# Optimization experiments

Measured on AMD Instinct MI355X. Metric: run time of the kernel, lower is better.

Reference implementation:

```python
import jax, jax.numpy as jnp
import numpy as np

B, H, W, C, NH, WS = 8, 113, 113, 512, 8, 7


def setup_inputs() -> dict:
    key = jax.random.key(0)
    k1, k2, k3 = jax.random.split(key, 3)
    x = jax.random.normal(k1, (B, H * W, C), jnp.float32)
    # torch Linear(embed_dims, 3*embed_dims, bias=False); stored as [C, 3C] for x @ W
    w_qkv = jax.random.normal(k2, (C, 3 * C), jnp.float32) * 0.02
    w_proj = jax.random.normal(k3, (C, C), jnp.float32) * 0.02
    b_proj = jnp.zeros((C,), jnp.float32)
    return {"x": x, "w_qkv": w_qkv, "w_proj": w_proj, "b_proj": b_proj, "h": H, "w": W}


def reference(x, w_qkv, w_proj, b_proj, h, w):
    b, n, c = x.shape
    ws, nh = WS, NH
    hd = c // nh
    scale = hd ** -0.5
    pad_b = (ws - h % ws) % ws
    pad_r = (ws - w % ws) % ws
    xi = x.reshape(b, h, w, c)
    xi = jnp.pad(xi, ((0, 0), (0, pad_b), (0, pad_r), (0, 0)))
    Hp, Wp = h + pad_b, w + pad_r
    _h, _w = Hp // ws, Wp // ws
    N = ws * ws
    nw = _h * _w

    # padding mask: 1 on padded rows/cols (matches torch fill of last pad_b rows / pad_r cols;
    # when pad==0 torch fills everything with 1 but mask differences are identically 0 either way)
    rows = jnp.arange(Hp)
    cols = jnp.arange(Wp)
    mask = ((rows[:, None] >= Hp - pad_b) | (cols[None, :] >= Wp - pad_r)).astype(x.dtype)
    mask = mask.reshape(_h, ws, _w, ws).transpose(0, 2, 1, 3).reshape(nw, N)
    am = mask[:, None, :] - mask[:, :, None]  # (nw, N, N)
    am = jnp.where(am != 0, jnp.asarray(-1000.0, x.dtype), jnp.asarray(0.0, x.dtype))

    # window partition: (b, _h, _w, ws, ws, c) -> (b, nw, N, c)
    xw = xi.reshape(b, _h, ws, _w, ws, c).transpose(0, 1, 3, 2, 4, 5).reshape(b, nw, N, c)

    qkv = (xw @ w_qkv).reshape(b, nw, N, 3, nh, hd)
    qkv = jnp.moveaxis(qkv, 3, 0)  # (3, b, nw, N, nh, hd)
    q = qkv[0].transpose(0, 1, 3, 2, 4)  # (b, nw, nh, N, hd)
    k = qkv[1].transpose(0, 1, 3, 2, 4)
    v = qkv[2].transpose(0, 1, 3, 2, 4)

    attn = jnp.einsum('bwhnd,bwhmd->bwhnm', q, k) * scale
    attn = attn + am[None, :, None, :, :]
    attn = jax.nn.softmax(attn, axis=-1)
    out = jnp.einsum('bwhnm,bwhmd->bwhnd', attn, v)  # (b, nw, nh, N, hd)

    # window merge back to (b, Hp, Wp, c)
    out = out.transpose(0, 1, 3, 2, 4).reshape(b, _h, _w, ws, ws, c)
    out = out.transpose(0, 1, 3, 2, 4, 5).reshape(b, Hp, Wp, c)
    out = out[:, :h, :w, :].reshape(b, n, c)
    return out @ w_proj + b_proj
```

## Files before the change

### kernel.cpp

```cpp
#include <hip/hip_runtime.h>
#include <hip/hip_fp16.h>
#include <stdint.h>

typedef _Float16 f16;
typedef __attribute__((ext_vector_type(4))) _Float16 f16x4;
typedef __attribute__((ext_vector_type(8))) _Float16 f16x8;
typedef __attribute__((ext_vector_type(4))) float f32x4;

#define DEVI static __device__ __forceinline__

#define C_DIM 512
#define M1    113288
#define M2    102152
#define NWIN  289
#define NTOK  49
#define NHW   18496
#define QKV_STRIDE 3136

DEVI void load_lds16(const f16* g, f16* l) {
  __builtin_amdgcn_global_load_lds((const __attribute__((address_space(1))) void*)g,
                                   (__attribute__((address_space(3))) void*)l,
                                   16, 0, 0);
}

DEVI f32x4 mfma_16x16x32(f16x8 a, f16x8 b, f32x4 c) {
  return __builtin_amdgcn_mfma_f32_16x16x32_f16(a, b, c, 0, 0, 0);
}

__global__ void cvt_x_kernel(const float* __restrict__ x, f16* __restrict__ xh,
                             f16* __restrict__ zp) {
  if (blockIdx.x == 0 && threadIdx.x < 64) {
    ((int4*)zp)[threadIdx.x] = make_int4(0, 0, 0, 0);
  }
  const int n8 = 6537728;
  int i = blockIdx.x * blockDim.x + threadIdx.x;
  for (; i < n8; i += gridDim.x * blockDim.x) {
    const float4* p = (const float4*)(x) + (size_t)i * 2;
    const float4 a = p[0], b = p[1];
    f16x8 o;
    o[0] = (f16)a.x; o[1] = (f16)a.y; o[2] = (f16)a.z; o[3] = (f16)a.w;
    o[4] = (f16)b.x; o[5] = (f16)b.y; o[6] = (f16)b.z; o[7] = (f16)b.w;
    *(f16x8*)(xh + (size_t)i * 8) = o;
  }
}

__global__ void cvt_wT_kernel(const float* __restrict__ w, f16* __restrict__ wt,
                              int K, int N) {
  const int i = blockIdx.x * blockDim.x + threadIdx.x;
  if (i < K * N) {
    const int n = i / K;
    const int k = i - n * K;
    wt[i] = (f16)w[(size_t)k * N + n];
  }
}

template<int MODE>
__global__ __launch_bounds__(256, 2)
void gemm_kernel(const f16* __restrict__ A, const f16* __restrict__ Bt,
                 f16* __restrict__ qo, f16* __restrict__ ko, f16* __restrict__ vo,
                 float* __restrict__ out, const float* __restrict__ bias,
                 const f16* __restrict__ zp)
{
  __shared__ __align__(16) f16 S[16384];
  f16* As = S;
  f16* Bs = S + 8192;

  const int tid  = threadIdx.x;
  const int wave = tid >> 6;
  const int lane = tid & 63;
  const int l16  = lane & 15;
  const int g    = lane >> 4;

  constexpr int NTN = (MODE == 0) ? 12 : 4;
  const int nwg = gridDim.x;
  const int qq = nwg >> 3, rr = nwg & 7;
  const int xcd = blockIdx.x & 7, ib = blockIdx.x >> 3;
  const int wg = (xcd < rr ? xcd * (qq + 1) : rr * (qq + 1) + (xcd - rr) * qq) + ib;
  const int tn = wg % NTN;
  const int tm = wg / NTN;

  const int srow  = tid >> 3;
  const int chunk = tid & 7;
  const int lc    = chunk ^ (srow & 7);
  const f16* asrc[4];
  const f16* bsrc[4];
  #pragma unroll
  for (int c = 0; c < 4; ++c) {
    const int m = tm * 128 + c * 32 + srow;
    long src = 0; bool valid;
    if (MODE == 0) {
      const int b   = m / 14161;
      const int rem = m - b * 14161;
      const int wi  = rem / 49;
      const int t   = rem - wi * 49;
      const int wh = wi / 17, ww = wi - (wi / 17) * 17;
      const int th = t / 7,   tw = t - (t / 7) * 7;
      const int h = wh * 7 + th, w = ww * 7 + tw;
      valid = (m < M1) && (h < 113) && (w < 113);
      src = (long)b * 12769 + h * 113 + w;
    } else {
      const int b = m / 12769;
      const int p = m - b * 12769;
      const int h = p / 113, w = p - (p / 113) * 113;
      valid = (m < M2);
      src = (long)((b * NWIN + (h / 7) * 17 + (w / 7)) * NTOK + (h % 7) * 7 + (w % 7));
    }
    asrc[c] = valid ? (A + src * C_DIM + lc * 8) : zp;
    bsrc[c] = Bt + (long)(tn * 128 + c * 32 + srow) * C_DIM + lc * 8;
  }

  int aoff[4], boff[4];
  #pragma unroll
  for (int i = 0; i < 4; ++i) {
    const int ra = (wave >> 1) * 64 + 16 * i + l16;
    aoff[i] = ra * 128 + ((g ^ (l16 & 7)) << 4);
    const int rb = (wave & 1) * 64 + 16 * i + l16;
    boff[i] = rb * 128 + ((g ^ (l16 & 7)) << 4);
  }

  f32x4 acc[4][4];
  #pragma unroll
  for (int i = 0; i < 4; ++i)
    #pragma unroll
    for (int j = 0; j < 4; ++j)
      acc[i][j] = (f32x4){0.f, 0.f, 0.f, 0.f};

  for (int kk = 0; kk < 8; ++kk) {
    __syncthreads();
    #pragma unroll
    for (int c = 0; c < 4; ++c) {
      load_lds16(asrc[c], &As[c * 2048 + wave * 512]);
      asrc[c] += 64;
    }
    #pragma unroll
    for (int c = 0; c < 4; ++c) {
      load_lds16(bsrc[c], &Bs[c * 2048 + wave * 512]);
      bsrc[c] += 64;
    }
    __syncthreads();

    #pragma unroll
    for (int kh = 0; kh < 2; ++kh) {
      f16x8 af[4], bf[4];
      #pragma unroll
      for (int i = 0; i < 4; ++i) af[i] = *(const f16x8*)((const char*)As + (aoff[i] ^ (kh << 6)));
      #pragma unroll
      for (int j = 0; j < 4; ++j) bf[j] = *(const f16x8*)((const char*)Bs + (boff[j] ^ (kh << 6)));
      #pragma unroll
      for (int i = 0; i < 4; ++i)
        #pragma unroll
        for (int j = 0; j < 4; ++j)
          acc[i][j] = mfma_16x16x32(af[i], bf[j], acc[i][j]);
    }
  }

  if (MODE == 0) {
    __syncthreads();
    char* Cs = (char*)S;
    const int rw0 = (wave >> 1) * 64 + g * 4;
    const int cl0 = (wave & 1) * 64 + l16;
    #pragma unroll
    for (int i = 0; i < 4; ++i) {
      #pragma unroll
      for (int rg = 0; rg < 4; ++rg) {
        const int row = rw0 + i * 16 + rg;
        const int xr  = ((row >> 2) & 3) << 5;
        #pragma unroll
        for (int j = 0; j < 4; ++j) {
          const int col = cl0 + j * 16;
          *(f16*)(Cs + row * 256 + ((col * 2) ^ xr)) = (f16)acc[i][j][rg];
        }
      }
    }
    __syncthreads();
    const int row  = tid >> 1;
    const int half = tid & 1;
    const int m = tm * 128 + row;
    if (m < M1) {
      const int bwi = m / 49;
      const int t   = m - bwi * 49;
      const int cwi = tn * 2 + half;
      f16* outw = (cwi < 8) ? qo : (cwi < 16) ? ko : vo;
      const int head = cwi & 7;
      f16* dst = outw + (size_t)(bwi * 8 + head) * QKV_STRIDE + t * 64;
      const int xr = ((row >> 2) & 3) << 5;
      #pragma unroll
      for (int c = 0; c < 8; ++c) {
        f16x8 v = *(const f16x8*)(Cs + row * 256 + ((half * 128 + c * 16) ^ xr));
        *(f16x8*)(dst + c * 8) = v;
      }
    }
  } else {
    const int rowb = tm * 128 + (wave >> 1) * 64 + g * 4;
    const int colb = tn * 128 + (wave & 1) * 64 + l16;
    #pragma unroll
    for (int i = 0; i < 4; ++i) {
      #pragma unroll
      for (int j = 0; j < 4; ++j) {
        const int col = colb + j * 16;
        const float bb = bias[col];
        #pragma unroll
        for (int rg = 0; rg < 4; ++rg) {
          const int m = rowb + i * 16 + rg;
          if (m < M2) out[(size_t)m * C_DIM + col] = acc[i][j][rg] + bb;
        }
      }
    }
  }
}

__global__ __launch_bounds__(256)
void attn_kernel(const f16* __restrict__ qg, const f16* __restrict__ kg,
                 const f16* __restrict__ vg, f16* __restrict__ og)
{
  __shared__ __align__(16) f16 plds[4][4096];
  __shared__ __align__(16) f16 vlds[4][2048];
  const int tid  = threadIdx.x;
  const int wv   = tid >> 6;
  const int lane = tid & 63;
  const int g    = lane >> 4;
  const int c    = lane & 15;
  const int hw   = blockIdx.x * 4 + wv;
  const int bwi  = hw >> 3;
  const int head = hw & 7;
  const int wi   = bwi % NWIN;
  const size_t bqk = (size_t)hw * QKV_STRIDE;
  const f16* vp = vg + (size_t)hw * QKV_STRIDE;

  f16x8 vreg[8];
  #pragma unroll
  for (int d0 = 0; d0 < 8; ++d0)
    vreg[d0] = *(const f16x8*)(vp + lane * 64 + d0 * 8);
  if (lane >= 49) {
    #pragma unroll
    for (int d0 = 0; d0 < 8; ++d0) vreg[d0] = (f16x8){};
  }

  const int wh = wi / 17, ww = wi - (wi / 17) * 17;
  unsigned long long pm = 0;
  if (wh == 16) pm |= (((1ull << 49) - 1) & ~0x7Full);
  if (ww == 16) {
    unsigned long long cm = 0;
    #pragma unroll
    for (int r7 = 0; r7 < 7; ++r7) cm |= 0x7Eull << (7 * r7);
    pm |= cm;
  }

  f32x4 acc[4][4];
  #pragma unroll
  for (int i = 0; i < 4; ++i)
    #pragma unroll
    for (int j = 0; j < 4; ++j) acc[i][j] = (f32x4){0.f, 0.f, 0.f, 0.f};

  const f16* kp = kg + bqk;
  const f16* qp = qg + bqk;
  #pragma unroll
  for (int s = 0; s < 2; ++s) {
    f16x8 kf[4], qf[4];
    #pragma unroll
    for (int i = 0; i < 4; ++i) kf[i] = *(const f16x8*)(kp + (16 * i + c) * 64 + 32 * s + 8 * g);
    #pragma unroll
    for (int j = 0; j < 4; ++j) qf[j] = *(const f16x8*)(qp + (16 * j + c) * 64 + 32 * s + 8 * g);
    #pragma unroll
    for (int i = 0; i < 4; ++i)
      #pragma unroll
      for (int j = 0; j < 4; ++j)
        acc[i][j] = mfma_16x16x32(kf[i], qf[j], acc[i][j]);
  }

  float invs[4];
  #pragma unroll
  for (int j = 0; j < 4; ++j) {
    const int q = 16 * j + c;
    const int padq = (int)((pm >> q) & 1);
    float sj = 0.f;
    #pragma unroll
    for (int i = 0; i < 4; ++i) {
      #pragma unroll
      for (int r = 0; r < 4; ++r) {
        const int key = 16 * i + 4 * g + r;
        const int padk = (int)((pm >> key) & 1);
        float sv = acc[i][j][r] * 0.125f + ((padk ^ padq) ? -1000.f : 0.f);
        float p = __expf(sv);
        if (i == 3) p = ((4 * g + r) == 0) ? p : 0.f;
        acc[i][j][r] = p;
        sj += p;
      }
    }
    invs[j] = sj;
  }
  #pragma unroll
  for (int j = 0; j < 4; ++j) {
    float sj = invs[j];
    sj += __shfl_xor(sj, 16);
    sj += __shfl_xor(sj, 32);
    invs[j] = 1.0f / sj;
  }

  f16* pl = &plds[wv][0];
  const int swz = (c & 7) << 4;
  #pragma unroll
  for (int j = 0; j < 4; ++j) {
    const int q = 16 * j + c;
    const float inv = invs[j];
    #pragma unroll
    for (int i = 0; i < 4; ++i) {
      f16x4 pk;
      pk[0] = (f16)(acc[i][j][0] * inv);
      pk[1] = (f16)(acc[i][j][1] * inv);
      pk[2] = (f16)(acc[i][j][2] * inv);
      pk[3] = (f16)(acc[i][j][3] * inv);
      *(f16x4*)((char*)pl + q * 128 + ((32 * i + 8 * g) ^ swz)) = pk;
    }
  }

  f16* vl = &vlds[wv][0];
  f32x4 o[4][4];
  #pragma unroll
  for (int i = 0; i < 4; ++i)
    #pragma unroll
    for (int j = 0; j < 4; ++j) o[i][j] = (f32x4){0.f, 0.f, 0.f, 0.f};

  #pragma unroll
  for (int h = 0; h < 2; ++h) {
    #pragma unroll
    for (int q4 = 0; q4 < 4; ++q4) {
      const int d0 = 4 * h + q4;
      #pragma unroll
      for (int j = 0; j < 8; ++j) {
        const int dr = (8 * d0 + j) & 31;
        *(f16*)((char*)vl + dr * 128 + ((lane * 2) ^ (j << 4))) = vreg[d0][j];
      }
    }
    #pragma unroll
    for (int s = 0; s < 2; ++s) {
      f16x8 vf[2], pf[4];
      #pragma unroll
      for (int n = 0; n < 2; ++n)
        vf[n] = *(const f16x8*)((const char*)vl + (16 * n + c) * 128 + ((64 * s + 16 * g) ^ swz));
      #pragma unroll
      for (int jq = 0; jq < 4; ++jq)
        pf[jq] = *(const f16x8*)((const char*)pl + (16 * jq + c) * 128 + ((64 * s + 16 * g) ^ swz));
      #pragma unroll
      for (int jq = 0; jq < 4; ++jq)
        #pragma unroll
        for (int n = 0; n < 2; ++n)
          o[jq][2 * h + n] = mfma_16x16x32(pf[jq], vf[n], o[jq][2 * h + n]);
    }
  }

  f16* ob = og + ((size_t)bwi * 49) * 512 + head * 64;
  #pragma unroll
  for (int jq = 0; jq < 4; ++jq) {
    #pragma unroll
    for (int r = 0; r < 4; ++r) {
      const int q = 16 * jq + 4 * g + r;
      if (q < 49) {
        #pragma unroll
        for (int n = 0; n < 4; ++n)
          ob[(size_t)q * 512 + 16 * n + c] = (f16)o[jq][n][r];
      }
    }
  }
}

extern "C" void kernel_launch(void* const* d_in, const int* in_sizes, int n_in,
                              void* d_out, int out_size, void* d_ws, size_t ws_size,
                              hipStream_t stream)
{
  const float* x     = (const float*)d_in[0];
  const float* wqkv  = (const float*)d_in[1];
  const float* wproj = (const float*)d_in[2];
  const float* bproj = (const float*)d_in[3];
  float* out = (float*)d_out;

  char* ws = (char*)d_ws;
  f16* zp = (f16*)ws;
  f16* xh = (f16*)(ws + 1024);
  f16* ah = xh;
  f16* qh = (f16*)(ws + 1024 + 116006912LL);
  f16* kh = qh + 58003456LL;
  f16* vh = kh + 58003456LL;
  f16* wqkvT  = vh + 58005504LL;
  f16* wprojT = wqkvT + 786432LL;

  cvt_x_kernel<<<2048, 256, 0, stream>>>(x, xh, zp);
  cvt_wT_kernel<<<(1536 * 512 + 255) / 256, 256, 0, stream>>>(wqkv, wqkvT, 512, 1536);
  cvt_wT_kernel<<<(512 * 512 + 255) / 256, 256, 0, stream>>>(wproj, wprojT, 512, 512);

  gemm_kernel<0><<<886 * 12, 256, 0, stream>>>(xh, wqkvT, qh, kh, vh, nullptr, nullptr, zp);

  attn_kernel<<<NHW / 4, 256, 0, stream>>>(qh, kh, vh, ah);

  gemm_kernel<1><<<799 * 4, 256, 0, stream>>>(ah, wprojT, nullptr, nullptr, nullptr, out, bproj, zp);
}
```

Before: 559.7 us.

## Fuse fp32-to-fp16 input conversion into the QKV GEMM A-tile load

Removes the standalone kernel that converted x to fp16 in the workspace. The QKV GEMM now reads fp32 x directly into registers, converts it to fp16 and writes it to LDS, with a register prefetch of the next K slice placed after the barrier. The aim is to eliminate a full extra read and write pass over the large activation tensor. In exchange, every N tile of the GEMM fetches twice as many A bytes as before, and the direct global-to-LDS loads are replaced by register-staged stores that raise register pressure.

```diff
diff --git a/kernel.cpp b/kernel.cpp
--- a/kernel.cpp
+++ b/kernel.cpp
@@ -27,21 +27,8 @@
   return __builtin_amdgcn_mfma_f32_16x16x32_f16(a, b, c, 0, 0, 0);
 }
 
-__global__ void cvt_x_kernel(const float* __restrict__ x, f16* __restrict__ xh,
-                             f16* __restrict__ zp) {
-  if (blockIdx.x == 0 && threadIdx.x < 64) {
-    ((int4*)zp)[threadIdx.x] = make_int4(0, 0, 0, 0);
-  }
-  const int n8 = 6537728;
-  int i = blockIdx.x * blockDim.x + threadIdx.x;
-  for (; i < n8; i += gridDim.x * blockDim.x) {
-    const float4* p = (const float4*)(x) + (size_t)i * 2;
-    const float4 a = p[0], b = p[1];
-    f16x8 o;
-    o[0] = (f16)a.x; o[1] = (f16)a.y; o[2] = (f16)a.z; o[3] = (f16)a.w;
-    o[4] = (f16)b.x; o[5] = (f16)b.y; o[6] = (f16)b.z; o[7] = (f16)b.w;
-    *(f16x8*)(xh + (size_t)i * 8) = o;
-  }
+__global__ void init_zp_kernel(f16* __restrict__ zp) {
+  ((int4*)zp)[threadIdx.x] = make_int4(0, 0, 0, 0);
 }
 
 __global__ void cvt_wT_kernel(const float* __restrict__ w, f16* __restrict__ wt,
@@ -56,7 +43,7 @@
 
 template<int MODE>
 __global__ __launch_bounds__(256, 2)
-void gemm_kernel(const f16* __restrict__ A, const f16* __restrict__ Bt,
+void gemm_kernel(const void* __restrict__ Asrc, const f16* __restrict__ Bt,
                  f16* __restrict__ qo, f16* __restrict__ ko, f16* __restrict__ vo,
                  float* __restrict__ out, const float* __restrict__ bias,
                  const f16* __restrict__ zp)
@@ -82,8 +69,12 @@
   const int srow  = tid >> 3;
   const int chunk = tid & 7;
   const int lc    = chunk ^ (srow & 7);
-  const f16* asrc[4];
+  const float* af32[4];
+  const f16*   a16[4];
   const f16* bsrc[4];
+  const float* xf  = (const float*)Asrc;
+  const f16*   ahp = (const f16*)Asrc;
+  const float* zpf = (const float*)zp;
   #pragma unroll
   for (int c = 0; c < 4; ++c) {
     const int m = tm * 128 + c * 32 + srow;
@@ -98,14 +89,15 @@
       const int h = wh * 7 + th, w = ww * 7 + tw;
       valid = (m < M1) && (h < 113) && (w < 113);
       src = (long)b * 12769 + h * 113 + w;
+      af32[c] = valid ? (xf + src * C_DIM + lc * 8) : zpf;
     } else {
       const int b = m / 12769;
       const int p = m - b * 12769;
       const int h = p / 113, w = p - (p / 113) * 113;
       valid = (m < M2);
       src = (long)((b * NWIN + (h / 7) * 17 + (w / 7)) * NTOK + (h % 7) * 7 + (w % 7));
-    }
-    asrc[c] = valid ? (A + src * C_DIM + lc * 8) : zp;
+      a16[c] = valid ? (ahp + src * C_DIM + lc * 8) : zp;
+    }
     bsrc[c] = Bt + (long)(tn * 128 + c * 32 + srow) * C_DIM + lc * 8;
   }
 
@@ -125,19 +117,55 @@
     for (int j = 0; j < 4; ++j)
       acc[i][j] = (f32x4){0.f, 0.f, 0.f, 0.f};
 
+  float4 ap[4][2];
+  if (MODE == 0) {
+    #pragma unroll
+    for (int c = 0; c < 4; ++c) {
+      const float4* p = (const float4*)af32[c];
+      ap[c][0] = p[0]; ap[c][1] = p[1];
+      af32[c] += 64;
+    }
+  }
+
   for (int kk = 0; kk < 8; ++kk) {
     __syncthreads();
-    #pragma unroll
-    for (int c = 0; c < 4; ++c) {
-      load_lds16(asrc[c], &As[c * 2048 + wave * 512]);
-      asrc[c] += 64;
-    }
-    #pragma unroll
-    for (int c = 0; c < 4; ++c) {
-      load_lds16(bsrc[c], &Bs[c * 2048 + wave * 512]);
-      bsrc[c] += 64;
-    }
-    __syncthreads();
+    if constexpr (MODE == 0) {
+      #pragma unroll
+      for (int c = 0; c < 4; ++c) {
+        load_lds16(bsrc[c], &Bs[c * 2048 + wave * 512]);
+        bsrc[c] += 64;
+      }
+      #pragma unroll
+      for (int c = 0; c < 4; ++c) {
+        f16x8 h;
+        h[0] = (f16)ap[c][0].x; h[1] = (f16)ap[c][0].y;
+        h[2] = (f16)ap[c][0].z; h[3] = (f16)ap[c][0].w;
+        h[4] = (f16)ap[c][1].x; h[5] = (f16)ap[c][1].y;
+        h[6] = (f16)ap[c][1].z; h[7] = (f16)ap[c][1].w;
+        *(f16x8*)(As + c * 2048 + tid * 8) = h;
+      }
+      __syncthreads();
+      if (kk < 7) {
+        #pragma unroll
+        for (int c = 0; c < 4; ++c) {
+          const float4* p = (const float4*)af32[c];
+          ap[c][0] = p[0]; ap[c][1] = p[1];
+          af32[c] += 64;
+        }
+      }
+    } else {
+      #pragma unroll
+      for (int c = 0; c < 4; ++c) {
+        load_lds16(a16[c], &As[c * 2048 + wave * 512]);
+        a16[c] += 64;
+      }
+      #pragma unroll
+      for (int c = 0; c < 4; ++c) {
+        load_lds16(bsrc[c], &Bs[c * 2048 + wave * 512]);
+        bsrc[c] += 64;
+      }
+      __syncthreads();
+    }
 
     #pragma unroll
     for (int kh = 0; kh < 2; ++kh) {
@@ -376,19 +404,18 @@
 
   char* ws = (char*)d_ws;
   f16* zp = (f16*)ws;
-  f16* xh = (f16*)(ws + 1024);
-  f16* ah = xh;
-  f16* qh = (f16*)(ws + 1024 + 116006912LL);
+  f16* ah = (f16*)(ws + 4096);
+  f16* qh = (f16*)(ws + 4096 + 116006912LL);
   f16* kh = qh + 58003456LL;
   f16* vh = kh + 58003456LL;
-  f16* wqkvT  = vh + 58005504LL;
+  f16* wqkvT  = vh + 58003456LL;
   f16* wprojT = wqkvT + 786432LL;
 
-  cvt_x_kernel<<<2048, 256, 0, stream>>>(x, xh, zp);
+  init_zp_kernel<<<1, 256, 0, stream>>>(zp);
   cvt_wT_kernel<<<(1536 * 512 + 255) / 256, 256, 0, stream>>>(wqkv, wqkvT, 512, 1536);
   cvt_wT_kernel<<<(512 * 512 + 255) / 256, 256, 0, stream>>>(wproj, wprojT, 512, 512);
 
-  gemm_kernel<0><<<886 * 12, 256, 0, stream>>>(xh, wqkvT, qh, kh, vh, nullptr, nullptr, zp);
+  gemm_kernel<0><<<886 * 12, 256, 0, stream>>>(x, wqkvT, qh, kh, vh, nullptr, nullptr, zp);
 
   attn_kernel<<<NHW / 4, 256, 0, stream>>>(qh, kh, vh, ah);
 
```

Measured after the change: 674.9 us. 20.6% more time.
